# Optimization experiments

Hardware: AMD Instinct MI355X
Metric: run time of the kernel (lower is better)

## Reference

```python
import jax, jax.numpy as jnp
import numpy as np

H, D = 4, 32
DIM = H * D      # hidden_dim * heads = 128
L = 2            # num_layers
F = 1000         # functions per graph
BINS = 16
T = 16           # tensor_neurons
BOTT = 16        # bottle_neck_neurons


def _hgt(xd, xi, especs, Wk, bk, Wq, bq, Wv, bv, Wa, ba, sk, ar, mr, pr):
    # One HGTConv: per-type K/Q/V linears, per-relation head matrices a_rel/m_rel,
    # joint segment-softmax over all incoming edges per dst node, sum-aggregate,
    # gelu -> per-type out linear -> sigmoid-skip residual.
    xt = {"data": xd, "inst": xi}
    Ns = {"data": xd.shape[0], "inst": xi.shape[0]}
    ti = {"data": 0, "inst": 1}

    def proj(W, b):
        return {t: (xt[t] @ W[ti[t]] + b[ti[t]]).reshape(Ns[t], H, D) for t in xt}

    k, q, v = proj(Wk, bk), proj(Wq, bq), proj(Wv, bv)
    buckets = {"data": [], "inst": []}
    for st, dt, ei, r in especs:
        src, dst = ei[0], ei[1]
        krel = jnp.einsum("ehd,hdf->ehf", k[st][src], ar[r])        # [E,H,D]
        logit = (q[dt][dst] * krel).sum(-1) * (pr[r] / (D ** 0.5))   # [E,H]
        vrel = jnp.einsum("ehd,hdf->ehf", v[st][src], mr[r])        # [E,H,D]
        buckets[dt].append((logit, dst, vrel))
    out = {}
    for t in ("data", "inst"):
        logits = jnp.concatenate([b[0] for b in buckets[t]], 0)
        dst = jnp.concatenate([b[1] for b in buckets[t]], 0)
        msgs = jnp.concatenate([b[2] for b in buckets[t]], 0)
        mx = jax.lax.stop_gradient(jax.ops.segment_max(logits, dst, num_segments=Ns[t]))
        e = jnp.exp(logits - mx[dst])
        den = jax.ops.segment_sum(e, dst, num_segments=Ns[t])
        w = e / jnp.maximum(den[dst], 1e-16)
        agg = jax.ops.segment_sum(msgs * w[..., None], dst, num_segments=Ns[t]).reshape(Ns[t], DIM)
        o = jax.nn.gelu(agg) @ Wa[ti[t]] + ba[ti[t]]
        s = jax.nn.sigmoid(sk[ti[t]])
        out[t] = s * o + (1.0 - s) * xt[t]
    return out["data"], out["inst"]


def _conv_pass(xd, xi, edges, P):
    Wk, bk, Wq, bq, Wv, bv, Wa, ba, sk, ar, mr, pr = P
    ec, ein, eou, eca = edges
    for l in range(L):
        fe = [("inst", "inst", ec, 0), ("data", "inst", ein, 1),
              ("inst", "data", eou, 2), ("inst", "inst", eca, 3)]
        re = [("inst", "inst", ec[::-1], 0), ("inst", "data", ein[::-1], 1),
              ("data", "inst", eou[::-1], 2), ("inst", "inst", eca[::-1], 3)]
        p0 = [A[l, 0] for A in (Wk, bk, Wq, bq, Wv, bv, Wa, ba, sk, ar, mr, pr)]
        p1 = [A[l, 1] for A in (Wk, bk, Wq, bq, Wv, bv, Wa, ba, sk, ar, mr, pr)]
        d1, i1 = _hgt(xd, xi, fe, *p0)
        d2, i2 = _hgt(xd, xi, re, *p1)
        xd = jax.nn.relu(0.5 * d1 + 0.5 * d2)   # alpha = 0.5
        xi = jax.nn.relu(0.5 * i1 + 0.5 * i2)
    return xd, xi


def _att_pool(x, W_att):
    # SimGNN AttentionModule
    c = jnp.tanh(jnp.mean(x @ W_att, axis=0))
    s = jax.nn.sigmoid(x @ c)
    return x.T @ s  # [DIM]


def _func_pool(xd, xi, fd, fi, W_att):
    # per-function attention pooling via segment ops (cat(data,inst) per function)
    x = jnp.concatenate([xd, xi], 0)
    f = jnp.concatenate([fd, fi], 0)
    sums = jax.ops.segment_sum(x @ W_att, f, num_segments=F)
    cnt = jax.ops.segment_sum(jnp.ones((x.shape[0],), jnp.float32), f, num_segments=F)
    c = jnp.tanh(sums / jnp.maximum(cnt, 1.0)[:, None])
    s = jax.nn.sigmoid((x * c[f]).sum(-1))
    return jax.ops.segment_sum(x * s[:, None], f, num_segments=F)  # [F,DIM]


def _forward(g1_x_data, g1_x_inst, g2_x_data, g2_x_inst, W_k, b_k, W_q, b_q, W_v, b_v,
             W_a, b_a, skip, a_rel, m_rel, p_rel, W_att, W_tn, V_tn, b_tn, W_fc1, b_fc1,
             W_sc, b_sc, g1_ei_control, g1_ei_input, g1_ei_output, g1_ei_call,
             g1_func_data, g1_func_inst, g2_ei_control, g2_ei_input, g2_ei_output,
             g2_ei_call, g2_func_data, g2_func_inst):
    P = (W_k, b_k, W_q, b_q, W_v, b_v, W_a, b_a, skip, a_rel, m_rel, p_rel)
    d1, i1 = _conv_pass(g1_x_data, g1_x_inst, (g1_ei_control, g1_ei_input, g1_ei_output, g1_ei_call), P)
    d2, i2 = _conv_pass(g2_x_data, g2_x_inst, (g2_ei_control, g2_ei_input, g2_ei_output, g2_ei_call), P)
    f1 = _func_pool(d1, i1, g1_func_data, g1_func_inst, W_att)
    f2 = _func_pool(d2, i2, g2_func_data, g2_func_inst, W_att)
    # histogram of detached similarity scores (torch.histc over [min,max])
    sc = jax.lax.stop_gradient(f1 @ f2.T).reshape(-1)
    mn, mx = sc.min(), sc.max()
    idx = jnp.clip(jnp.floor((sc - mn) / jnp.maximum(mx - mn, 1e-12) * BINS).astype(jnp.int32), 0, BINS - 1)
    hist = jax.ops.segment_sum(jnp.ones_like(sc), idx, num_segments=BINS)
    hist = hist / hist.sum()
    p1 = _att_pool(jnp.concatenate([d1, i1], 0), W_att)
    p2 = _att_pool(jnp.concatenate([d2, i2], 0), W_att)
    scoring = jnp.einsum("i,ijk,j->k", p1, W_tn, p2)          # NTN bilinear [T]
    block = V_tn @ jnp.concatenate([p1, p2]) + b_tn
    tnet = jax.nn.relu(scoring + block)
    feats = jnp.concatenate([tnet, hist])[None, :]             # [1, T+BINS]
    h = jax.nn.relu(feats @ W_fc1 + b_fc1)
    return jax.nn.sigmoid(h @ W_sc + b_sc)                     # [1,1]


def setup_inputs():
    key = jax.random.key(0)
    ks = iter(jax.random.split(key, 80))
    Nd, Ni = 30000, 60000
    Ec, Ein, Eou, Eca = 120000, 90000, 90000, 30000

    def nrm(shape, s):
        return jax.random.normal(next(ks), shape, jnp.float32) * s

    def ri(n, hi):
        return jax.random.randint(next(ks), (n,), 0, hi, jnp.int32)

    inp = {}
    for g in ("g1", "g2"):
        inp[g + "_x_data"] = nrm((Nd, DIM), 1.0)
        inp[g + "_x_inst"] = nrm((Ni, DIM), 1.0)
        inp[g + "_ei_control"] = jnp.stack([ri(Ec, Ni), ri(Ec, Ni)])
        inp[g + "_ei_input"] = jnp.stack([ri(Ein, Nd), ri(Ein, Ni)])
        inp[g + "_ei_output"] = jnp.stack([ri(Eou, Ni), ri(Eou, Nd)])
        inp[g + "_ei_call"] = jnp.stack([ri(Eca, Ni), ri(Eca, Ni)])
        inp[g + "_func_data"] = (jnp.arange(Nd) % F).astype(jnp.int32)
        inp[g + "_func_inst"] = (jnp.arange(Ni) % F).astype(jnp.int32)
    w = 1.0 / (DIM ** 0.5)
    for nm in ("k", "q", "v", "a"):
        inp["W_" + nm] = nrm((L, 2, 2, DIM, DIM), w)
        inp["b_" + nm] = jnp.zeros((L, 2, 2, DIM), jnp.float32)
    inp["skip"] = jnp.ones((L, 2, 2), jnp.float32)
    inp["a_rel"] = nrm((L, 2, 4, H, D, D), 1.0 / (D ** 0.5))
    inp["m_rel"] = nrm((L, 2, 4, H, D, D), 1.0 / (D ** 0.5))
    inp["p_rel"] = jnp.ones((L, 2, 4, H), jnp.float32)
    inp["W_att"] = nrm((DIM, DIM), w)
    inp["W_tn"] = nrm((DIM, DIM, T), w)
    inp["V_tn"] = nrm((T, 2 * DIM), w)
    inp["b_tn"] = jnp.zeros((T,), jnp.float32)
    inp["W_fc1"] = nrm((T + BINS, BOTT), 0.1)
    inp["b_fc1"] = jnp.zeros((BOTT,), jnp.float32)
    inp["W_sc"] = nrm((BOTT, 1), 0.1)
    inp["b_sc"] = jnp.zeros((1,), jnp.float32)
    return inp


def reference(g1_x_data, g1_x_inst, g2_x_data, g2_x_inst, W_k, b_k, W_q, b_q, W_v, b_v,
              W_a, b_a, skip, a_rel, m_rel, p_rel, W_att, W_tn, V_tn, b_tn, W_fc1, b_fc1,
              W_sc, b_sc, g1_ei_control, g1_ei_input, g1_ei_output, g1_ei_call,
              g1_func_data, g1_func_inst, g2_ei_control, g2_ei_input, g2_ei_output,
              g2_ei_call, g2_func_data, g2_func_inst):
    return _forward(g1_x_data, g1_x_inst, g2_x_data, g2_x_inst, W_k, b_k, W_q, b_q, W_v, b_v,
                    W_a, b_a, skip, a_rel, m_rel, p_rel, W_att, W_tn, V_tn, b_tn, W_fc1, b_fc1,
                    W_sc, b_sc, g1_ei_control, g1_ei_input, g1_ei_output, g1_ei_call,
                    g1_func_data, g1_func_inst, g2_ei_control, g2_ei_input, g2_ei_output,
                    g2_ei_call, g2_func_data, g2_func_inst)
```

## Files before the change

### kernel.cpp

```cpp
#include <hip/hip_runtime.h>
#include <math.h>

#define FFUNC 1000

typedef __attribute__((ext_vector_type(8))) short s8v;
typedef __attribute__((ext_vector_type(4))) float f4v;

__device__ __forceinline__ float sigf(float x){ return 1.0f/(1.0f+__expf(-x)); }
__device__ __forceinline__ float geluf(float x){
  float u = 1.5957691216057308f * (x + 0.044715f*x*x*x);
  return x / (1.0f + __expf(-u));
}
__device__ __forceinline__ unsigned fkey(float f){
  unsigned u = __float_as_uint(f);
  return (u & 0x80000000u) ? ~u : (u | 0x80000000u);
}
__device__ __forceinline__ float funkey(unsigned k){
  unsigned u = (k & 0x80000000u) ? (k ^ 0x80000000u) : ~k;
  return __uint_as_float(u);
}
__device__ __forceinline__ void atomAddF(float* p, float v){ unsafeAtomicAdd(p, v); }
__device__ __forceinline__ unsigned short bfr(float x){
  unsigned u = __float_as_uint(x);
  unsigned r = (u + 0x7FFFu + ((u >> 16) & 1u)) >> 16;
  return (unsigned short)r;
}
__device__ __forceinline__ float b2f(unsigned short v){
  return __uint_as_float((unsigned)v << 16);
}

__global__ void packw_k(const float* __restrict__ W, unsigned short* __restrict__ out){
  int mat = blockIdx.x;
  const float* w = W + (size_t)mat*16384;
  unsigned short* o = out + (size_t)mat*16384;
  for (int u=0; u<64; u++){
    int oi = u*256 + threadIdx.x;
    int j = oi & 7, l = (oi>>3) & 63, nt = (oi>>9) & 7, kt = oi >> 12;
    float v = w[(size_t)(kt*32 + 8*(l>>4) + j)*128 + nt*16 + (l&15)];
    o[oi] = bfr(v);
  }
}

__global__ void packa_k(const float* __restrict__ A, unsigned short* __restrict__ out){
  int ent = blockIdx.x;
  const float* a = A + (size_t)ent*4096;
  unsigned short* o = out + (size_t)ent*4096;
  for (int u=0; u<16; u++){
    int oi = u*256 + threadIdx.x;
    int j = oi & 7, l = (oi>>3) & 63, nt = (oi>>9) & 1, h = oi >> 10;
    float v = a[(size_t)h*1024 + (size_t)(8*(l>>4)+j)*32 + nt*16 + (l&15)];
    o[oi] = bfr(v);
  }
}

struct KX { int styp[4]; int koff[4]; };
__global__ __launch_bounds__(256) void gemm_kqvx_k(
    const void* __restrict__ xdv, const void* __restrict__ xiv, int af32,
    int nd, int ni, int gbd,
    const unsigned short* __restrict__ WK, const unsigned short* __restrict__ WQ,
    const unsigned short* __restrict__ WV,
    const float* __restrict__ bK, const float* __restrict__ bQ, const float* __restrict__ bV,
    const unsigned short* __restrict__ ARpc, const unsigned short* __restrict__ MRpc,
    unsigned short* __restrict__ Qb,
    unsigned short* __restrict__ KRK, unsigned short* __restrict__ KRV, KX kx)
{
  __shared__ __align__(16) unsigned short tile[64*128];
  int blk = blockIdx.x;
  int ty = (blk >= gbd);
  int N = ty ? ni : nd;
  int rbase = (ty ? (blk - gbd) : blk) * 64;
  size_t obase = ty ? (size_t)nd*128 : 0;
  const unsigned short* wk = WK + (ty ? 16384 : 0);
  const unsigned short* wq = WQ + (ty ? 16384 : 0);
  const unsigned short* wv = WV + (ty ? 16384 : 0);
  const float* bk2 = bK + (ty ? 128 : 0);
  const float* bq2 = bQ + (ty ? 128 : 0);
  const float* bv2 = bV + (ty ? 128 : 0);
  const float* Af = (const float*)(ty ? xiv : xdv);
  const unsigned short* Ab = (const unsigned short*)(ty ? xiv : xdv);

  int t = threadIdx.x;
  int l = t & 63, w = t >> 6, b = l >> 4, m = l & 15;
  int arow = rbase + w*16 + m;
  bool rv = arow < N;
  int lrow = w*16 + m;

  s8v axf[4];
  #pragma unroll
  for (int kt=0; kt<4; kt++){
    s8v af = (s8v){0,0,0,0,0,0,0,0};
    if (rv){
      if (af32){
        const float* ap = Af + (size_t)arow*128 + kt*32 + b*8;
        float4 x0 = *(const float4*)ap;
        float4 x1 = *(const float4*)(ap + 4);
        af[0]=(short)bfr(x0.x); af[1]=(short)bfr(x0.y); af[2]=(short)bfr(x0.z); af[3]=(short)bfr(x0.w);
        af[4]=(short)bfr(x1.x); af[5]=(short)bfr(x1.y); af[6]=(short)bfr(x1.z); af[7]=(short)bfr(x1.w);
      } else {
        af = *(const s8v*)(Ab + (size_t)arow*128 + kt*32 + b*8);
      }
    }
    axf[kt] = af;
  }

  f4v acc[8];
  #pragma unroll
  for (int nt=0; nt<8; nt++) acc[nt] = (f4v){0,0,0,0};
  #pragma unroll
  for (int kt=0; kt<4; kt++)
    #pragma unroll
    for (int nt=0; nt<8; nt++){
      s8v bf = *(const s8v*)(wq + ((kt*8 + nt)*64 + l)*8);
      acc[nt] = __builtin_amdgcn_mfma_f32_16x16x32_bf16(axf[kt], bf, acc[nt], 0, 0, 0);
    }
  #pragma unroll
  for (int r2=0; r2<4; r2++){
    int trow = w*16 + 4*b + r2;
    #pragma unroll
    for (int nt=0; nt<8; nt++){
      int col = nt*16 + m;
      int ch = (col>>3) ^ (trow&15);
      tile[trow*128 + ch*8 + (col&7)] = bfr(acc[nt][r2] + bq2[col]);
    }
  }
  __syncthreads();
  #pragma unroll
  for (int it=0; it<4; it++){
    int idx = it*256 + t;
    int rr = idx >> 4, cc = idx & 15;
    int orow = rbase + rr;
    if (orow < N)
      *(uint4*)(Qb + obase + (size_t)orow*128 + cc*8) =
          *(const uint4*)(&tile[rr*128 + ((cc ^ (rr&15))*8)]);
  }
  __syncthreads();

  #pragma unroll
  for (int nt=0; nt<8; nt++) acc[nt] = (f4v){0,0,0,0};
  #pragma unroll
  for (int kt=0; kt<4; kt++)
    #pragma unroll
    for (int nt=0; nt<8; nt++){
      s8v bf = *(const s8v*)(wk + ((kt*8 + nt)*64 + l)*8);
      acc[nt] = __builtin_amdgcn_mfma_f32_16x16x32_bf16(axf[kt], bf, acc[nt], 0, 0, 0);
    }
  #pragma unroll
  for (int r2=0; r2<4; r2++){
    int trow = w*16 + 4*b + r2;
    #pragma unroll
    for (int nt=0; nt<8; nt++){
      int col = nt*16 + m;
      int ch = (col>>3) ^ (trow&15);
      tile[trow*128 + ch*8 + (col&7)] = bfr(acc[nt][r2] + bk2[col]);
    }
  }
  __syncthreads();
  {
    s8v kf[4];
    #pragma unroll
    for (int h=0; h<4; h++){
      int ch = (h*4 + b) ^ (lrow&15);
      kf[h] = *(const s8v*)(&tile[lrow*128 + ch*8]);
    }
    __syncthreads();
    #pragma unroll
    for (int r=0; r<4; r++){
      if (kx.styp[r] != ty) continue;
      const unsigned short* Ap = ARpc + r*4096;
      f4v xa[8];
      #pragma unroll
      for (int i=0;i<8;i++) xa[i] = (f4v){0,0,0,0};
      #pragma unroll
      for (int h=0; h<4; h++)
        #pragma unroll
        for (int n2=0; n2<2; n2++){
          s8v bf = *(const s8v*)(Ap + ((h*2 + n2)*64 + l)*8);
          xa[h*2+n2] = __builtin_amdgcn_mfma_f32_16x16x32_bf16(kf[h], bf, xa[h*2+n2], 0, 0, 0);
        }
      #pragma unroll
      for (int r2=0; r2<4; r2++){
        int trow = w*16 + 4*b + r2;
        #pragma unroll
        for (int h=0; h<4; h++)
          #pragma unroll
          for (int n2=0; n2<2; n2++){
            int col = h*32 + n2*16 + m;
            int ch = (col>>3) ^ (trow&15);
            tile[trow*128 + ch*8 + (col&7)] = bfr(xa[h*2+n2][r2]);
          }
      }
      __syncthreads();
      int ko = kx.koff[r];
      #pragma unroll
      for (int it=0; it<4; it++){
        int idx = it*256 + t;
        int rr = idx >> 4, cc = idx & 15;
        int orow = rbase + rr;
        if (orow < N)
          *(uint4*)(KRK + (size_t)(ko + orow)*128 + cc*8) =
              *(const uint4*)(&tile[rr*128 + ((cc ^ (rr&15))*8)]);
      }
      __syncthreads();
    }
  }

  #pragma unroll
  for (int nt=0; nt<8; nt++) acc[nt] = (f4v){0,0,0,0};
  #pragma unroll
  for (int kt=0; kt<4; kt++)
    #pragma unroll
    for (int nt=0; nt<8; nt++){
      s8v bf = *(const s8v*)(wv + ((kt*8 + nt)*64 + l)*8);
      acc[nt] = __builtin_amdgcn_mfma_f32_16x16x32_bf16(axf[kt], bf, acc[nt], 0, 0, 0);
    }
  #pragma unroll
  for (int r2=0; r2<4; r2++){
    int trow = w*16 + 4*b + r2;
    #pragma unroll
    for (int nt=0; nt<8; nt++){
      int col = nt*16 + m;
      int ch = (col>>3) ^ (trow&15);
      tile[trow*128 + ch*8 + (col&7)] = bfr(acc[nt][r2] + bv2[col]);
    }
  }
  __syncthreads();
  {
    s8v vf[4];
    #pragma unroll
    for (int h=0; h<4; h++){
      int ch = (h*4 + b) ^ (lrow&15);
      vf[h] = *(const s8v*)(&tile[lrow*128 + ch*8]);
    }
    __syncthreads();
    #pragma unroll
    for (int r=0; r<4; r++){
      if (kx.styp[r] != ty) continue;
      const unsigned short* Ap = MRpc + r*4096;
      f4v xa[8];
      #pragma unroll
      for (int i=0;i<8;i++) xa[i] = (f4v){0,0,0,0};
      #pragma unroll
      for (int h=0; h<4; h++)
        #pragma unroll
        for (int n2=0; n2<2; n2++){
          s8v bf = *(const s8v*)(Ap + ((h*2 + n2)*64 + l)*8);
          xa[h*2+n2] = __builtin_amdgcn_mfma_f32_16x16x32_bf16(vf[h], bf, xa[h*2+n2], 0, 0, 0);
        }
      #pragma unroll
      for (int r2=0; r2<4; r2++){
        int trow = w*16 + 4*b + r2;
        #pragma unroll
        for (int h=0; h<4; h++)
          #pragma unroll
          for (int n2=0; n2<2; n2++){
            int col = h*32 + n2*16 + m;
            int ch = (col>>3) ^ (trow&15);
            tile[trow*128 + ch*8 + (col&7)] = bfr(xa[h*2+n2][r2]);
          }
      }
      __syncthreads();
      int ko = kx.koff[r];
      #pragma unroll
      for (int it=0; it<4; it++){
        int idx = it*256 + t;
        int rr = idx >> 4, cc = idx & 15;
        int orow = rbase + rr;
        if (orow < N)
          *(uint4*)(KRV + (size_t)(ko + orow)*128 + cc*8) =
              *(const uint4*)(&tile[rr*128 + ((cc ^ (rr&15))*8)]);
      }
      __syncthreads();
    }
  }
}

__global__ __launch_bounds__(256) void gemm_epi_k(
    const unsigned short* __restrict__ AGGb, const float* __restrict__ DENb,
    int nd, int ni, int gbd,
    const unsigned short* __restrict__ WA, const float* __restrict__ bA,
    const void* __restrict__ xin_dv, const void* __restrict__ xin_iv, int xf32,
    const unsigned short* __restrict__ o1p, unsigned short* __restrict__ out,
    const float* __restrict__ skp, int mode)
{
  __shared__ __align__(16) float ftile[64*128];
  int blk = blockIdx.x;
  int ty = (blk >= gbd);
  int N = ty ? ni : nd;
  int rbase = (ty ? (blk - gbd) : blk) * 64;
  int goff = ty ? nd : 0;
  const unsigned short* wa = WA + (ty ? 16384 : 0);
  const float* ba2 = bA + (ty ? 128 : 0);
  const float* xinF = (const float*)(ty ? xin_iv : xin_dv);
  const unsigned short* xinB = (const unsigned short*)(ty ? xin_iv : xin_dv);
  float s = sigf(skp[ty]), s1 = 1.0f - s;

  int t = threadIdx.x;
  int l = t & 63, w = t >> 6, b = l >> 4, m = l & 15;
  int arow = rbase + w*16 + m;
  bool rv = arow < N;
  f4v acc[8];
  #pragma unroll
  for (int nt=0; nt<8; nt++) acc[nt] = (f4v){0,0,0,0};

  float4 dv4 = make_float4(1.f,1.f,1.f,1.f);
  if (rv){
    size_t grow = (size_t)(goff + arow);
    float4 dr = *(const float4*)(DENb + grow*4);
    dv4.x = 1.0f / fmaxf(dr.x, 1e-16f);
    dv4.y = 1.0f / fmaxf(dr.y, 1e-16f);
    dv4.z = 1.0f / fmaxf(dr.z, 1e-16f);
    dv4.w = 1.0f / fmaxf(dr.w, 1e-16f);
  }
  #pragma unroll
  for (int kt=0; kt<4; kt++){
    s8v af = (s8v){0,0,0,0,0,0,0,0};
    if (rv){
      size_t grow = (size_t)(goff + arow);
      float dv = (kt==0)?dv4.x:(kt==1)?dv4.y:(kt==2)?dv4.z:dv4.w;
      s8v ag = *(const s8v*)(AGGb + grow*128 + kt*32 + b*8);
      #pragma unroll
      for (int jj=0; jj<8; jj++)
        af[jj] = (short)bfr(geluf(b2f((unsigned short)ag[jj]) * dv));
    }
    #pragma unroll
    for (int nt=0; nt<8; nt++){
      s8v bf = *(const s8v*)(wa + ((kt*8 + nt)*64 + l)*8);
      acc[nt] = __builtin_amdgcn_mfma_f32_16x16x32_bf16(af, bf, acc[nt], 0, 0, 0);
    }
  }
  #pragma unroll
  for (int r2=0; r2<4; r2++){
    int trow = w*16 + 4*b + r2;
    #pragma unroll
    for (int nt=0; nt<8; nt++){
      int col = nt*16 + m;
      int ch = (col>>2) ^ (trow&31);
      ftile[trow*128 + ch*4 + (col&3)] = acc[nt][r2];
    }
  }
  __syncthreads();
  #pragma unroll
  for (int it=0; it<8; it++){
    int idx = it*256 + t;
    int rr = idx >> 5, cc = idx & 31;
    int orow = rbase + rr;
    if (orow >= N) continue;
    size_t grow = (size_t)(goff + orow);
    float4 a4 = *(const float4*)(&ftile[rr*128 + ((cc ^ (rr&31))*4)]);
    float4 b4 = *(const float4*)(ba2 + cc*4);
    float xv0, xv1, xv2, xv3;
    if (xf32){
      float4 x4 = *(const float4*)(xinF + (size_t)orow*128 + cc*4);
      xv0=x4.x; xv1=x4.y; xv2=x4.z; xv3=x4.w;
    } else {
      ushort4 x4 = *(const ushort4*)(xinB + (size_t)orow*128 + cc*4);
      xv0=b2f(x4.x); xv1=b2f(x4.y); xv2=b2f(x4.z); xv3=b2f(x4.w);
    }
    float v0 = s*(a4.x + b4.x) + s1*xv0;
    float v1 = s*(a4.y + b4.y) + s1*xv1;
    float v2 = s*(a4.z + b4.z) + s1*xv2;
    float v3 = s*(a4.w + b4.w) + s1*xv3;
    if (mode == 3){
      ushort4 o4 = *(const ushort4*)(o1p + grow*128 + cc*4);
      v0 = fmaxf(0.5f*b2f(o4.x) + 0.5f*v0, 0.f);
      v1 = fmaxf(0.5f*b2f(o4.y) + 0.5f*v1, 0.f);
      v2 = fmaxf(0.5f*b2f(o4.z) + 0.5f*v2, 0.f);
      v3 = fmaxf(0.5f*b2f(o4.w) + 0.5f*v3, 0.f);
    }
    *(ushort4*)(out + grow*128 + cc*4) =
        make_ushort4(bfr(v0), bfr(v1), bfr(v2), bfr(v3));
  }
}

struct ScanDesc { int n[8]; };

struct HD {
  int blk0[9];
  const int* dst[8];
  const int* src[8];
  int E[8];
  int cnto[8];
  int permo[8];
};
__global__ void csr_hist_all_k(HD d, int* __restrict__ cnt){
  int b = blockIdx.x;
  int r = 0;
  while (r < 7 && b >= d.blk0[r+1]) r++;
  int e = (b - d.blk0[r])*256 + threadIdx.x;
  if (e < d.E[r]) atomicAdd(&cnt[d.cnto[r] + d.dst[r][e]], 1);
}
__global__ void csr_fill_all_k(HD d, int* __restrict__ curs, int* __restrict__ perm){
  int b = blockIdx.x;
  int r = 0;
  while (r < 7 && b >= d.blk0[r+1]) r++;
  int e = (b - d.blk0[r])*256 + threadIdx.x;
  if (e < d.E[r]){
    int pos = atomicAdd(&curs[d.cnto[r] + d.dst[r][e]], 1);
    perm[d.permo[r] + pos] = d.src[r][e] | ((r & 3) << 24);
  }
}

__global__ __launch_bounds__(1024) void scan_p1(ScanDesc sd, const int* __restrict__ offs,
                                                int* __restrict__ part, int NO, int MAXT){
  int ent = blockIdx.y, tile = blockIdx.x;
  int n = sd.n[ent];
  int i = tile*1024 + threadIdx.x;
  int v = (i < n) ? offs[(size_t)ent*NO + i] : 0;
  #pragma unroll
  for (int d2=1; d2<64; d2<<=1) v += __shfl_xor(v, d2, 64);
  __shared__ int ws_[16];
  int lane = threadIdx.x & 63, wv = threadIdx.x >> 6;
  if (lane == 0) ws_[wv] = v;
  __syncthreads();
  if (threadIdx.x == 0){
    int s = 0;
    #pragma unroll
    for (int k=0;k<16;k++) s += ws_[k];
    part[ent*MAXT + tile] = s;
  }
}

__global__ __launch_bounds__(1024) void scan_p2(int* __restrict__ part, int MAXT, int nent){
  int tid = threadIdx.x, lane = tid & 63, wv = tid >> 6;
  __shared__ int wsum[16];
  __shared__ int woff[17];
// ... 296 lines not shown
        mn = fminf(mn, v); mx = fmaxf(mx, v);
      }
    }
  }
  __shared__ float smn[256], smx[256];
  smn[t]=mn; smx[t]=mx; __syncthreads();
  for (int o=128;o>0;o>>=1){
    if (t<o){ smn[t]=fminf(smn[t],smn[t+o]); smx[t]=fmaxf(smx[t],smx[t+o]); }
    __syncthreads();
  }
  if (t==0){ atomicMin(&mmk[0], fkey(smn[0])); atomicMax(&mmk[1], fkey(smx[0])); }
}

__global__ void hist_init_k(unsigned* mmk, unsigned* hist){
  int t = threadIdx.x;
  if (t==0){ mmk[0]=0xFFFFFFFFu; mmk[1]=0u; }
  if (t<16) hist[t]=0u;
}

__global__ void hist_k(const float* __restrict__ sc, const unsigned* __restrict__ mmk,
                       unsigned* __restrict__ hist)
{
  __shared__ unsigned hl[16];
  int t = threadIdx.x;
  if (t < 16) hl[t] = 0;
  __syncthreads();
  float mn = funkey(mmk[0]), mx = funkey(mmk[1]);
  float rng = fmaxf(mx - mn, 1e-12f);
  const long total = (long)FFUNC*FFUNC;
  for (long idx = (long)blockIdx.x*256 + t; idx < total; idx += (long)gridDim.x*256){
    float v = sc[idx];
    int b = (int)floorf((v - mn)/rng * 16.0f);
    b = min(max(b,0),15);
    atomicAdd(&hl[b], 1u);
  }
  __syncthreads();
  if (t < 16) atomicAdd(&hist[t], hl[t]);
}

__global__ __launch_bounds__(256) void final_k(
    const float* __restrict__ p1, const float* __restrict__ p2,
    const float* __restrict__ Wtn, const float* __restrict__ Vtn,
    const float* __restrict__ btn, const unsigned* __restrict__ hist,
    const float* __restrict__ Wfc1, const float* __restrict__ bfc1,
    const float* __restrict__ Wsc, const float* __restrict__ bsc,
    float* __restrict__ outp)
{
  __shared__ float P1[128], P2[128], part[256], feats[32], hv[16];
  int t = threadIdx.x;
  if (t < 128){ P1[t] = p1[t]; P2[t] = p2[t]; }
  __syncthreads();
  int k = t & 15, pr_ = t >> 4;
  float acc = 0;
  for (int i = pr_*8; i < pr_*8+8; ++i){
    float pi = P1[i];
    const float* wrow = Wtn + ((size_t)i*128)*16 + k;
    float a2 = 0;
    for (int j=0;j<128;++j) a2 += P2[j]*wrow[(size_t)j*16];
    acc += pi*a2;
  }
  part[t] = acc;
  __syncthreads();
  if (t < 16){
    float sc_ = 0;
    for (int p=0;p<16;p++) sc_ += part[p*16 + t];
    float bl = btn[t];
    for (int j=0;j<256;j++) bl += Vtn[(size_t)t*256 + j] * (j<128 ? P1[j] : P2[j-128]);
    float tv = sc_ + bl;
    feats[t] = tv > 0.f ? tv : 0.f;
    feats[16+t] = (float)hist[t] * (1.0f/((float)FFUNC*(float)FFUNC));
  }
  __syncthreads();
  if (t < 16){
    float a2 = bfc1[t];
    for (int q2=0;q2<32;q2++) a2 += feats[q2]*Wfc1[q2*16 + t];
    hv[t] = a2 > 0.f ? a2 : 0.f;
  }
  __syncthreads();
  if (t == 0){
    float z = bsc[0];
    for (int m=0;m<16;m++) z += hv[m]*Wsc[m];
    outp[0] = sigf(z);
  }
}

extern "C" void kernel_launch(void* const* d_in, const int* in_sizes, int n_in,
                              void* d_out, int out_size, void* d_ws, size_t ws_size,
                              hipStream_t stream)
{
  (void)n_in; (void)out_size; (void)ws_size;
  const float* Wk = (const float*)d_in[16];
  const float* bk = (const float*)d_in[17];
  const float* Wq = (const float*)d_in[18];
  const float* bq = (const float*)d_in[19];
  const float* Wv = (const float*)d_in[20];
  const float* bv = (const float*)d_in[21];
  const float* Wa = (const float*)d_in[22];
  const float* ba = (const float*)d_in[23];
  const float* SKp = (const float*)d_in[24];
  const float* AR = (const float*)d_in[25];
  const float* MRm = (const float*)d_in[26];
  const float* PRp = (const float*)d_in[27];
  const float* WATT = (const float*)d_in[28];
  const float* WTN = (const float*)d_in[29];
  const float* VTN = (const float*)d_in[30];
  const float* BTN = (const float*)d_in[31];
  const float* WFC1 = (const float*)d_in[32];
  const float* BFC1 = (const float*)d_in[33];
  const float* WSC = (const float*)d_in[34];
  const float* BSC = (const float*)d_in[35];

  int NdA[2] = { in_sizes[0]/128, in_sizes[8]/128 };
  int NiA[2] = { in_sizes[1]/128, in_sizes[9]/128 };
  int EA[2][4];
  for (int g=0; g<2; g++)
    for (int r=0; r<4; r++) EA[g][r] = in_sizes[g*8+2+r]/2;

  int NdM = NdA[0] > NdA[1] ? NdA[0] : NdA[1];
  int NiM = NiA[0] > NiA[1] ? NiA[0] : NiA[1];
  long EtotM = 0;
  for (int g=0; g<2; g++){
    long et = 0; for (int r=0;r<4;r++) et += EA[g][r];
    if (et > EtotM) EtotM = et;
  }
  size_t nrowsM = (size_t)NdM + (size_t)NiM;
  int NOR = (int)(((nrowsM + 2 + 63)/64)*64);
  long KR4rows = 3L*NiM + NdM;

  char* wp = (char*)d_ws;
  auto alloc = [&](size_t bytes)->void*{
    void* p = (void*)wp;
    wp += (bytes + 255) & ~(size_t)255;
    return p;
  };
  unsigned short* Xb   = (unsigned short*)alloc(nrowsM*128*2);
  unsigned short* AGGb = (unsigned short*)alloc(nrowsM*128*2);
  float*          DEN  = (float*)alloc(nrowsM*4*4);
  unsigned short* O1b  = (unsigned short*)alloc(nrowsM*128*2);
  unsigned short* Qb   = (unsigned short*)alloc(nrowsM*128*2);
  unsigned short* KRK  = (unsigned short*)alloc((size_t)KR4rows*128*2);
  unsigned short* KRV  = (unsigned short*)alloc((size_t)KR4rows*128*2);
  int*            OFFS3= (int*)alloc((size_t)3*NOR*4);
  int*            PERM = (int*)alloc((size_t)2*EtotM*4);
  int*            FPERM= (int*)alloc(nrowsM*4);
  int*            PART = (int*)alloc((size_t)3*1024*4);
  float*          GS[2];
  GS[0] = (float*)alloc((size_t)257280*4);
  GS[1] = (float*)alloc((size_t)257280*4);
  unsigned short* FB[2];
  FB[0] = (unsigned short*)alloc((size_t)FFUNC*128*2);
  FB[1] = (unsigned short*)alloc((size_t)FFUNC*128*2);
  unsigned*       MM   = (unsigned*)alloc(2*4);
  unsigned*       HIST = (unsigned*)alloc(16*4);
  unsigned short* WKP  = (unsigned short*)alloc((size_t)8*16384*2);
  unsigned short* WQP  = (unsigned short*)alloc((size_t)8*16384*2);
  unsigned short* WVP  = (unsigned short*)alloc((size_t)8*16384*2);
  unsigned short* WAP  = (unsigned short*)alloc((size_t)8*16384*2);
  unsigned short* WATTP= (unsigned short*)alloc((size_t)16384*2);
  unsigned short* ARP  = (unsigned short*)alloc((size_t)16*4096*2);
  unsigned short* MRP  = (unsigned short*)alloc((size_t)16*4096*2);
  size_t uni_bytes = (size_t)FFUNC*FFUNC*4;
  size_t curs_bytes = (size_t)3*NOR*4;
  void* UNI = alloc(uni_bytes > curs_bytes ? uni_bytes : curs_bytes);
  int*   CURS3 = (int*)UNI;
  float* SCb   = (float*)UNI;

  packw_k<<<8,256,0,stream>>>(Wk, WKP);
  packw_k<<<8,256,0,stream>>>(Wq, WQP);
  packw_k<<<8,256,0,stream>>>(Wv, WVP);
  packw_k<<<8,256,0,stream>>>(Wa, WAP);
  packw_k<<<1,256,0,stream>>>(WATT, WATTP);
  packa_k<<<16,256,0,stream>>>(AR, ARP);
  packa_k<<<16,256,0,stream>>>(MRm, MRP);

  const size_t OF_FSUM=0, OF_FCNT=128000, OF_CF=129024, OF_ATTC=257024, OF_POOL=257152;
  const int stf[4] = {1,0,1,1};
  const int dtf[4] = {1,1,0,1};

  for (int g=0; g<2; ++g){
    int nd = NdA[g], ni = NiA[g];
    int nrows = nd + ni;
    int E[4] = {EA[g][0],EA[g][1],EA[g][2],EA[g][3]};
    const int* ei[4] = {(const int*)d_in[g*8+2], (const int*)d_in[g*8+3],
                        (const int*)d_in[g*8+4], (const int*)d_in[g*8+5]};
    const int* fdp = (const int*)d_in[g*8+6];
    const int* fip = (const int*)d_in[g*8+7];
    const float* x0d = (const float*)d_in[g*8+0];
    const float* x0i = (const float*)d_in[g*8+1];
    int gbd = (nd+63)/64, gbi = (ni+63)/64;
    int nb = gbd + gbi;
    int ntb = (nrows+255)/256; if (ntb > 2048) ntb = 2048;

    int koff[2][4], stA[2][4], dtA[2][4];
    for (int c=0;c<2;c++){
      int run = 0;
      for (int r=0;r<4;r++){
        stA[c][r] = (c==0) ? stf[r] : dtf[r];
        dtA[c][r] = (c==0) ? dtf[r] : stf[r];
        koff[c][r] = run;
        run += stA[c][r] ? ni : nd;
      }
    }

    hipMemsetAsync(OFFS3, 0, (size_t)3*NOR*4, stream);
    HD hd; int hb = 0;
    for (int c2=0; c2<2; c2++)
      for (int r=0; r<4; r++){
        int ent = c2*4 + r;
        hd.blk0[ent] = hb;
        hd.dst[ent] = (c2==0) ? ei[r]+E[r] : ei[r];
        hd.src[ent] = (c2==0) ? ei[r] : ei[r]+E[r];
        hd.E[ent] = E[r];
        hd.cnto[ent] = c2*NOR + (dtA[c2][r] ? nd : 0);
        hd.permo[ent] = c2*(int)EtotM;
        hb += (E[r]+255)/256;
      }
    hd.blk0[8] = hb;
    csr_hist_all_k<<<hb,256,0,stream>>>(hd, OFFS3);
    fhist_k<<<ntb,256,0,stream>>>(fdp, fip, nd, ni, OFFS3 + (size_t)2*NOR);
    ScanDesc sd; sd.n[0] = nrows; sd.n[1] = nrows; sd.n[2] = FFUNC;
    int maxtiles = (nrows + 1023)/1024; if (maxtiles < 1) maxtiles = 1;
    dim3 sgrid(maxtiles, 3);
    scan_p1<<<sgrid,1024,0,stream>>>(sd, OFFS3, PART, NOR, maxtiles);
    scan_p2<<<1,1024,0,stream>>>(PART, maxtiles, 3);
    scan_p3<<<sgrid,1024,0,stream>>>(sd, OFFS3, CURS3, PART, NOR, maxtiles);
    csr_fill_all_k<<<hb,256,0,stream>>>(hd, CURS3, PERM);
    ffill_k<<<ntb,256,0,stream>>>(fdp, fip, nd, ni, CURS3 + (size_t)2*NOR, FPERM);

    for (int l=0; l<2; ++l){
      const void* xd = (l==0) ? (const void*)x0d : (const void*)Xb;
      const void* xi = (l==0) ? (const void*)x0i : (const void*)(Xb + (size_t)nd*128);
      int af32 = (l==0);
      for (int c=0; c<2; ++c){
        int pc = l*2 + c;
        KX kx;
        for (int r=0;r<4;r++){ kx.styp[r] = stA[c][r]; kx.koff[r] = koff[c][r]; }
        gemm_kqvx_k<<<nb,256,0,stream>>>(
            xd, xi, af32, nd, ni, gbd,
            WKP+(size_t)pc*2*16384, WQP+(size_t)pc*2*16384, WVP+(size_t)pc*2*16384,
            bk+(size_t)pc*2*128, bq+(size_t)pc*2*128, bv+(size_t)pc*2*128,
            ARP + (size_t)pc*4*4096, MRP + (size_t)pc*4*4096,
            Qb, KRK, KRV, kx);
        MD md;
        for (int r=0;r<4;r++) md.koff[r] = koff[c][r];
        int eblk = (nrows*32 + 255)/256;
        e12m_k<<<eblk,256,0,stream>>>(KRK, KRV, Qb,
                                      OFFS3 + (size_t)c*NOR, PERM + (size_t)c*EtotM, nrows,
                                      PRp + (size_t)pc*16, AGGb, DEN, md);
        gemm_epi_k<<<nb,256,0,stream>>>(
            AGGb, DEN, nd, ni, gbd,
            WAP+(size_t)pc*2*16384, ba+(size_t)pc*2*128,
            xd, xi, af32,
            (c==1) ? O1b : (const unsigned short*)nullptr,
            (c==0) ? O1b : Xb,
            SKp + (size_t)pc*2, (c==0) ? 2 : 3);
      }
    }
    float* fsum = GS[g]+OF_FSUM;  float* fcnt = GS[g]+OF_FCNT;
    float* cf   = GS[g]+OF_CF;    float* attc = GS[g]+OF_ATTC;
    float* pool = GS[g]+OF_POOL;
    hipMemsetAsync(pool, 0, 128*4, stream);
    f1c_k<<<FFUNC,256,0,stream>>>(Xb, OFFS3 + (size_t)2*NOR, FPERM, fsum, fcnt);
    attc2_k<<<1,1024,0,stream>>>(fsum, 1.0f/(float)nrows, WATT, attc);
    gemmb_k<<<(FFUNC+63)/64,256,0,stream>>>(fsum, FFUNC, WATTP, nullptr, cf, 1, fcnt);
    f23c_k<<<FFUNC,256,0,stream>>>(Xb, OFFS3 + (size_t)2*NOR, FPERM, cf, attc, FB[g], pool);
  }
  hist_init_k<<<1,32,0,stream>>>(MM, HIST);
  dim3 gnt((FFUNC+63)/64, (FFUNC+63)/64);
  gemmnt_b<<<gnt,256,0,stream>>>(FB[0], FB[1], SCb, MM);
  hist_k<<<512,256,0,stream>>>(SCb, MM, HIST);
  final_k<<<1,256,0,stream>>>(GS[0]+OF_POOL, GS[1]+OF_POOL, WTN, VTN, BTN, HIST,
                              WFC1, BFC1, WSC, BSC, (float*)d_out);
}
```

Baseline: 1.764 ms.

## Precompose K/V projections with relation matrices into composite per-relation weights

Adds a setup kernel that folds each relation's a_rel/m_rel head matrices into the K and V projection weights and biases, giving one composite 128x128 bf16 weight per relation. The projection kernel then runs a generic loop of full GEMMs per output (Q plus K-rel and V-rel per relation) with a double-buffered shared tile. This removes the intermediate K/V round trip through shared memory, the second chain of small block-diagonal MFMAs and several barriers. In exchange it does more MFMA work per relation, since the block-diagonal structure is lost, and it adds a one-time setup kernel.

```diff
diff --git a/kernel.cpp b/kernel.cpp
--- a/kernel.cpp
+++ b/kernel.cpp
@@ -41,41 +41,56 @@
   }
 }
 
-__global__ void packa_k(const float* __restrict__ A, unsigned short* __restrict__ out){
-  int ent = blockIdx.x;
-  const float* a = A + (size_t)ent*4096;
-  unsigned short* o = out + (size_t)ent*4096;
-  for (int u=0; u<16; u++){
+__global__ __launch_bounds__(256) void comp_k(
+    const float* __restrict__ Wk, const float* __restrict__ bk,
+    const float* __restrict__ Wv, const float* __restrict__ bv,
+    const float* __restrict__ AR, const float* __restrict__ MR,
+    unsigned short* __restrict__ OC, float* __restrict__ OB)
+{
+  const int stf[4]={1,0,1,1}, dtf[4]={1,1,0,1};
+  int b = blockIdx.x, kv = b>>5, idx = b&31, pcc = idx>>2, r = idx&3;
+  int pc = pcc>>1, c = pcc&1;
+  int styp = (c==0) ? stf[r] : dtf[r];
+  const float* W  = (kv ? Wv : Wk) + (size_t)(pc*2+styp)*16384;
+  const float* bi = (kv ? bv : bk) + (size_t)(pc*2+styp)*128;
+  const float* a  = (kv ? MR : AR) + (size_t)(pc*4+r)*4096;
+  unsigned short* oc = OC + (size_t)b*16384;
+  float* ob = OB + (size_t)b*128;
+  __shared__ float as[4096];
+  for (int i=threadIdx.x; i<4096; i+=256) as[i] = a[i];
+  __syncthreads();
+  for (int u=0; u<64; u++){
     int oi = u*256 + threadIdx.x;
-    int j = oi & 7, l = (oi>>3) & 63, nt = (oi>>9) & 1, h = oi >> 10;
-    float v = a[(size_t)h*1024 + (size_t)(8*(l>>4)+j)*32 + nt*16 + (l&15)];
-    o[oi] = bfr(v);
-  }
-}
-
-struct KX { int styp[4]; int koff[4]; };
-__global__ __launch_bounds__(256) void gemm_kqvx_k(
+    int j = oi&7, l = (oi>>3)&63, nt = (oi>>9)&7, kt = oi>>12;
+    int k = kt*32 + 8*(l>>4) + j;
+    int col = nt*16 + (l&15);
+    int h = col>>5, f = col&31;
+    const float* wr = W + (size_t)k*128 + h*32;
+    const float* ap = as + h*1024 + f;
+    float s = 0;
+    #pragma unroll 8
+    for (int d=0; d<32; d++) s += wr[d]*ap[d*32];
+    oc[oi] = bfr(s);
+  }
+  if (threadIdx.x < 128){
+    int col = threadIdx.x, h = col>>5, f = col&31;
+    float s = 0;
+    for (int d=0; d<32; d++) s += bi[h*32+d]*as[h*1024 + d*32 + f];
+    ob[col] = s;
+  }
+}
+
+struct OutD { const unsigned short* w; const float* bi; unsigned short* dst; };
+struct KSet { int nout; OutD o[7]; };
+__global__ __launch_bounds__(256) void gemm_kqvc_k(
     const void* __restrict__ xdv, const void* __restrict__ xiv, int af32,
-    int nd, int ni, int gbd,
-    const unsigned short* __restrict__ WK, const unsigned short* __restrict__ WQ,
-    const unsigned short* __restrict__ WV,
-    const float* __restrict__ bK, const float* __restrict__ bQ, const float* __restrict__ bV,
-    const unsigned short* __restrict__ ARpc, const unsigned short* __restrict__ MRpc,
-    unsigned short* __restrict__ Qb,
-    unsigned short* __restrict__ KRK, unsigned short* __restrict__ KRV, KX kx)
-{
-  __shared__ __align__(16) unsigned short tile[64*128];
+    int nd, int ni, int gbd, KSet kd, KSet ki)
+{
+  __shared__ __align__(16) unsigned short tile[2][64*128];
   int blk = blockIdx.x;
   int ty = (blk >= gbd);
   int N = ty ? ni : nd;
   int rbase = (ty ? (blk - gbd) : blk) * 64;
-  size_t obase = ty ? (size_t)nd*128 : 0;
-  const unsigned short* wk = WK + (ty ? 16384 : 0);
-  const unsigned short* wq = WQ + (ty ? 16384 : 0);
-  const unsigned short* wv = WV + (ty ? 16384 : 0);
-  const float* bk2 = bK + (ty ? 128 : 0);
-  const float* bq2 = bQ + (ty ? 128 : 0);
-  const float* bv2 = bV + (ty ? 128 : 0);
   const float* Af = (const float*)(ty ? xiv : xdv);
   const unsigned short* Ab = (const unsigned short*)(ty ? xiv : xdv);
 
@@ -83,7 +98,6 @@
   int l = t & 63, w = t >> 6, b = l >> 4, m = l & 15;
   int arow = rbase + w*16 + m;
   bool rv = arow < N;
-  int lrow = w*16 + m;
 
   s8v axf[4];
   #pragma unroll
@@ -103,174 +117,43 @@
     axf[kt] = af;
   }
 
-  f4v acc[8];
-  #pragma unroll
-  for (int nt=0; nt<8; nt++) acc[nt] = (f4v){0,0,0,0};
-  #pragma unroll
-  for (int kt=0; kt<4; kt++)
-    #pragma unroll
-    for (int nt=0; nt<8; nt++){
-      s8v bf = *(const s8v*)(wq + ((kt*8 + nt)*64 + l)*8);
-      acc[nt] = __builtin_amdgcn_mfma_f32_16x16x32_bf16(axf[kt], bf, acc[nt], 0, 0, 0);
-    }
-  #pragma unroll
-  for (int r2=0; r2<4; r2++){
-    int trow = w*16 + 4*b + r2;
-    #pragma unroll
-    for (int nt=0; nt<8; nt++){
-      int col = nt*16 + m;
-      int ch = (col>>3) ^ (trow&15);
-      tile[trow*128 + ch*8 + (col&7)] = bfr(acc[nt][r2] + bq2[col]);
-    }
-  }
-  __syncthreads();
-  #pragma unroll
-  for (int it=0; it<4; it++){
-    int idx = it*256 + t;
-    int rr = idx >> 4, cc = idx & 15;
-    int orow = rbase + rr;
-    if (orow < N)
-      *(uint4*)(Qb + obase + (size_t)orow*128 + cc*8) =
-          *(const uint4*)(&tile[rr*128 + ((cc ^ (rr&15))*8)]);
-  }
-  __syncthreads();
-
-  #pragma unroll
-  for (int nt=0; nt<8; nt++) acc[nt] = (f4v){0,0,0,0};
-  #pragma unroll
-  for (int kt=0; kt<4; kt++)
-    #pragma unroll
-    for (int nt=0; nt<8; nt++){
-      s8v bf = *(const s8v*)(wk + ((kt*8 + nt)*64 + l)*8);
-      acc[nt] = __builtin_amdgcn_mfma_f32_16x16x32_bf16(axf[kt], bf, acc[nt], 0, 0, 0);
-    }
-  #pragma unroll
-  for (int r2=0; r2<4; r2++){
-    int trow = w*16 + 4*b + r2;
-    #pragma unroll
-    for (int nt=0; nt<8; nt++){
-      int col = nt*16 + m;
-      int ch = (col>>3) ^ (trow&15);
-      tile[trow*128 + ch*8 + (col&7)] = bfr(acc[nt][r2] + bk2[col]);
-    }
-  }
-  __syncthreads();
-  {
-    s8v kf[4];
-    #pragma unroll
-    for (int h=0; h<4; h++){
-      int ch = (h*4 + b) ^ (lrow&15);
-      kf[h] = *(const s8v*)(&tile[lrow*128 + ch*8]);
+  int nout = ty ? ki.nout : kd.nout;
+  int cur = 0;
+  for (int i=0; i<nout; i++){
+    const unsigned short* wp = ty ? ki.o[i].w   : kd.o[i].w;
+    const float*          bi = ty ? ki.o[i].bi  : kd.o[i].bi;
+    unsigned short*      dst = ty ? ki.o[i].dst : kd.o[i].dst;
+    f4v acc[8];
+    #pragma unroll
+    for (int nt=0; nt<8; nt++) acc[nt] = (f4v){0,0,0,0};
+    #pragma unroll
+    for (int kt=0; kt<4; kt++)
+      #pragma unroll
+      for (int nt=0; nt<8; nt++){
+        s8v bf = *(const s8v*)(wp + ((kt*8 + nt)*64 + l)*8);
+        acc[nt] = __builtin_amdgcn_mfma_f32_16x16x32_bf16(axf[kt], bf, acc[nt], 0, 0, 0);
+      }
+    #pragma unroll
+    for (int r2=0; r2<4; r2++){
+      int trow = w*16 + 4*b + r2;
+      #pragma unroll
+      for (int nt=0; nt<8; nt++){
+        int col = nt*16 + m;
+        int ch = (col>>3) ^ (trow&15);
+        tile[cur][trow*128 + ch*8 + (col&7)] = bfr(acc[nt][r2] + bi[col]);
+      }
     }
     __syncthreads();
     #pragma unroll
-    for (int r=0; r<4; r++){
-      if (kx.styp[r] != ty) continue;
-      const unsigned short* Ap = ARpc + r*4096;
-      f4v xa[8];
-      #pragma unroll
-      for (int i=0;i<8;i++) xa[i] = (f4v){0,0,0,0};
-      #pragma unroll
-      for (int h=0; h<4; h++)
-        #pragma unroll
-        for (int n2=0; n2<2; n2++){
-          s8v bf = *(const s8v*)(Ap + ((h*2 + n2)*64 + l)*8);
-          xa[h*2+n2] = __builtin_amdgcn_mfma_f32_16x16x32_bf16(kf[h], bf, xa[h*2+n2], 0, 0, 0);
-        }
-      #pragma unroll
-      for (int r2=0; r2<4; r2++){
-        int trow = w*16 + 4*b + r2;
-        #pragma unroll
-        for (int h=0; h<4; h++)
-          #pragma unroll
-          for (int n2=0; n2<2; n2++){
-            int col = h*32 + n2*16 + m;
-            int ch = (col>>3) ^ (trow&15);
-            tile[trow*128 + ch*8 + (col&7)] = bfr(xa[h*2+n2][r2]);
-          }
-      }
-      __syncthreads();
-      int ko = kx.koff[r];
-      #pragma unroll
-      for (int it=0; it<4; it++){
-        int idx = it*256 + t;
-        int rr = idx >> 4, cc = idx & 15;
-        int orow = rbase + rr;
-        if (orow < N)
-          *(uint4*)(KRK + (size_t)(ko + orow)*128 + cc*8) =
-              *(const uint4*)(&tile[rr*128 + ((cc ^ (rr&15))*8)]);
-      }
-      __syncthreads();
-    }
-  }
-
-  #pragma unroll
-  for (int nt=0; nt<8; nt++) acc[nt] = (f4v){0,0,0,0};
-  #pragma unroll
-  for (int kt=0; kt<4; kt++)
-    #pragma unroll
-    for (int nt=0; nt<8; nt++){
-      s8v bf = *(const s8v*)(wv + ((kt*8 + nt)*64 + l)*8);
-      acc[nt] = __builtin_amdgcn_mfma_f32_16x16x32_bf16(axf[kt], bf, acc[nt], 0, 0, 0);
-    }
-  #pragma unroll
-  for (int r2=0; r2<4; r2++){
-    int trow = w*16 + 4*b + r2;
-    #pragma unroll
-    for (int nt=0; nt<8; nt++){
-      int col = nt*16 + m;
-      int ch = (col>>3) ^ (trow&15);
-      tile[trow*128 + ch*8 + (col&7)] = bfr(acc[nt][r2] + bv2[col]);
-    }
-  }
-  __syncthreads();
-  {
-    s8v vf[4];
-    #pragma unroll
-    for (int h=0; h<4; h++){
-      int ch = (h*4 + b) ^ (lrow&15);
-      vf[h] = *(const s8v*)(&tile[lrow*128 + ch*8]);
-    }
-    __syncthreads();
-    #pragma unroll
-    for (int r=0; r<4; r++){
-      if (kx.styp[r] != ty) continue;
-      const unsigned short* Ap = MRpc + r*4096;
-      f4v xa[8];
-      #pragma unroll
-      for (int i=0;i<8;i++) xa[i] = (f4v){0,0,0,0};
-      #pragma unroll
-      for (int h=0; h<4; h++)
-        #pragma unroll
-        for (int n2=0; n2<2; n2++){
-          s8v bf = *(const s8v*)(Ap + ((h*2 + n2)*64 + l)*8);
-          xa[h*2+n2] = __builtin_amdgcn_mfma_f32_16x16x32_bf16(vf[h], bf, xa[h*2+n2], 0, 0, 0);
-        }
-      #pragma unroll
-      for (int r2=0; r2<4; r2++){
-        int trow = w*16 + 4*b + r2;
-        #pragma unroll
-        for (int h=0; h<4; h++)
-          #pragma unroll
-          for (int n2=0; n2<2; n2++){
-            int col = h*32 + n2*16 + m;
-            int ch = (col>>3) ^ (trow&15);
-            tile[trow*128 + ch*8 + (col&7)] = bfr(xa[h*2+n2][r2]);
-          }
-      }
-      __syncthreads();
-      int ko = kx.koff[r];
-      #pragma unroll
-      for (int it=0; it<4; it++){
-        int idx = it*256 + t;
-        int rr = idx >> 4, cc = idx & 15;
-        int orow = rbase + rr;
-        if (orow < N)
-          *(uint4*)(KRV + (size_t)(ko + orow)*128 + cc*8) =
-              *(const uint4*)(&tile[rr*128 + ((cc ^ (rr&15))*8)]);
-      }
-      __syncthreads();
-    }
+    for (int it=0; it<4; it++){
+      int idx = it*256 + t;
+      int rr = idx >> 4, cc = idx & 15;
+      int orow = rbase + rr;
+      if (orow < N)
+        *(uint4*)(dst + (size_t)orow*128 + cc*8) =
+            *(const uint4*)(&tile[cur][rr*128 + ((cc ^ (rr&15))*8)]);
+    }
+    cur ^= 1;
   }
 }
 
@@ -873,26 +756,21 @@
   FB[1] = (unsigned short*)alloc((size_t)FFUNC*128*2);
   unsigned*       MM   = (unsigned*)alloc(2*4);
   unsigned*       HIST = (unsigned*)alloc(16*4);
-  unsigned short* WKP  = (unsigned short*)alloc((size_t)8*16384*2);
   unsigned short* WQP  = (unsigned short*)alloc((size_t)8*16384*2);
-  unsigned short* WVP  = (unsigned short*)alloc((size_t)8*16384*2);
   unsigned short* WAP  = (unsigned short*)alloc((size_t)8*16384*2);
   unsigned short* WATTP= (unsigned short*)alloc((size_t)16384*2);
-  unsigned short* ARP  = (unsigned short*)alloc((size_t)16*4096*2);
-  unsigned short* MRP  = (unsigned short*)alloc((size_t)16*4096*2);
+  unsigned short* COMPX= (unsigned short*)alloc((size_t)64*16384*2);
+  float*          BCX  = (float*)alloc((size_t)64*128*4);
   size_t uni_bytes = (size_t)FFUNC*FFUNC*4;
   size_t curs_bytes = (size_t)3*NOR*4;
   void* UNI = alloc(uni_bytes > curs_bytes ? uni_bytes : curs_bytes);
   int*   CURS3 = (int*)UNI;
   float* SCb   = (float*)UNI;
 
-  packw_k<<<8,256,0,stream>>>(Wk, WKP);
   packw_k<<<8,256,0,stream>>>(Wq, WQP);
-  packw_k<<<8,256,0,stream>>>(Wv, WVP);
   packw_k<<<8,256,0,stream>>>(Wa, WAP);
   packw_k<<<1,256,0,stream>>>(WATT, WATTP);
-  packa_k<<<16,256,0,stream>>>(AR, ARP);
-  packa_k<<<16,256,0,stream>>>(MRm, MRP);
+  comp_k<<<64,256,0,stream>>>(Wk, bk, Wv, bv, AR, MRm, COMPX, BCX);
 
   const size_t OF_FSUM=0, OF_FCNT=128000, OF_CF=129024, OF_ATTC=257024, OF_POOL=257152;
   const int stf[4] = {1,0,1,1};
@@ -954,14 +832,27 @@
       int af32 = (l==0);
       for (int c=0; c<2; ++c){
         int pc = l*2 + c;
-        KX kx;
-        for (int r=0;r<4;r++){ kx.styp[r] = stA[c][r]; kx.koff[r] = koff[c][r]; }
-        gemm_kqvx_k<<<nb,256,0,stream>>>(
-            xd, xi, af32, nd, ni, gbd,
-            WKP+(size_t)pc*2*16384, WQP+(size_t)pc*2*16384, WVP+(size_t)pc*2*16384,
-            bk+(size_t)pc*2*128, bq+(size_t)pc*2*128, bv+(size_t)pc*2*128,
-            ARP + (size_t)pc*4*4096, MRP + (size_t)pc*4*4096,
-            Qb, KRK, KRV, kx);
+        KSet kd, ki;
+        kd.nout = 1; ki.nout = 1;
+        kd.o[0].w = WQP + (size_t)(pc*2+0)*16384;
+        kd.o[0].bi = bq + (size_t)(pc*2+0)*128;
+        kd.o[0].dst = Qb;
+        ki.o[0].w = WQP + (size_t)(pc*2+1)*16384;
+        ki.o[0].bi = bq + (size_t)(pc*2+1)*128;
+        ki.o[0].dst = Qb + (size_t)nd*128;
+        for (int r=0;r<4;r++){
+          int cid = (pc*2+c)*4 + r;
+          KSet& ks = stA[c][r] ? ki : kd;
+          ks.o[ks.nout].w = COMPX + (size_t)cid*16384;
+          ks.o[ks.nout].bi = BCX + (size_t)cid*128;
+          ks.o[ks.nout].dst = KRK + (size_t)koff[c][r]*128;
+          ks.nout++;
+          ks.o[ks.nout].w = COMPX + (size_t)(32+cid)*16384;
+          ks.o[ks.nout].bi = BCX + (size_t)(32+cid)*128;
+          ks.o[ks.nout].dst = KRV + (size_t)koff[c][r]*128;
+          ks.nout++;
+        }
+        gemm_kqvc_k<<<nb,256,0,stream>>>(xd, xi, af32, nd, ni, gbd, kd, ki);
         MD md;
         for (int r=0;r<4;r++) md.koff[r] = koff[c][r];
         int eblk = (nrows*32 + 255)/256;
```

After: 1.606 ms. 8.9% less time.
